# Performance work log

Hardware: AMD Instinct MI355X
Metric: run time of the kernel (lower is better)

The kernel has to match this reference:

```python
import jax, jax.numpy as jnp
import numpy as np

NEG_SLOPE = 0.2
EPS = 1e-16


def _add_self_loops(edge_index, edge_weight, N):
    # PyG add_self_loops with fill_value='mean': self-loop attr = mean of
    # incoming edge attrs per node (0 if node has no incoming edges).
    src, dst = edge_index[0], edge_index[1]
    ones = jnp.ones_like(edge_weight)
    cnt = jax.ops.segment_sum(ones, dst, num_segments=N)
    wsum = jax.ops.segment_sum(edge_weight, dst, num_segments=N)
    self_w = jnp.where(cnt > 0, wsum / jnp.maximum(cnt, 1.0), 0.0)
    loop = jnp.arange(N, dtype=src.dtype)
    return (jnp.concatenate([src, loop]), jnp.concatenate([dst, loop]),
            jnp.concatenate([edge_weight, self_w]))


def _gatv2_layer(x, src, dst, ew, Wl, Wr, att, We, bias, N):
    # x: [M, N, Din]; src/dst: [E']; ew: [E']; att: [H, C]
    M = x.shape[0]
    H, C = att.shape
    xl = (x @ Wl).reshape(M, N, H, C)   # source transform (lin_l)
    xr = (x @ Wr).reshape(M, N, H, C)   # target transform (lin_r)
    xj = xl[:, src]                      # [M, E', H, C] gather source feats
    xi = xr[:, dst]                      # [M, E', H, C] gather target feats
    ee = (ew[:, None] @ We).reshape(-1, H, C)  # [E', H, C] edge embedding
    s = jax.nn.leaky_relu(xi + xj + ee[None], NEG_SLOPE)
    logits = jnp.einsum('mehc,hc->meh', s, att)  # [M, E', H]
    # segment softmax over edges grouped by destination node
    smax = jax.vmap(lambda u: jax.ops.segment_max(u, dst, num_segments=N))(logits)
    a = jnp.exp(logits - smax[:, dst])
    denom = jax.vmap(lambda u: jax.ops.segment_sum(u, dst, num_segments=N))(a)
    alpha = a / (denom[:, dst] + EPS)
    msg = alpha[..., None] * xj          # [M, E', H, C]
    out = jax.vmap(lambda u: jax.ops.segment_sum(u, dst, num_segments=N))(msg)
    return out.reshape(M, N, H * C) + bias


def setup_inputs() -> dict:
    key = jax.random.key(0)
    ks = jax.random.split(key, 14)
    B, T, N, Din = 2, 8, 5000, 64
    E, H, OUT = 80000, 2, 128
    C = OUT // H  # 64
    g = jax.nn.initializers.glorot_uniform()
    inp = {
        'x': jax.random.normal(ks[0], (B, T, N, Din), jnp.float32),
        'edge_index': jax.random.randint(ks[1], (2, E), 0, N, jnp.int32),
        'edge_weight': jax.random.uniform(ks[2], (E,), jnp.float32),
        # conv1 params
        'Wl1': g(ks[3], (Din, H * C), jnp.float32),
        'Wr1': g(ks[4], (Din, H * C), jnp.float32),
        'att1': g(ks[5], (H, C), jnp.float32),
        'We1': g(ks[6], (1, H * C), jnp.float32),
        'b1': jnp.zeros((H * C,), jnp.float32),
        # conv2 params
        'Wl2': g(ks[7], (OUT, H * C), jnp.float32),
        'Wr2': g(ks[8], (OUT, H * C), jnp.float32),
        'att2': g(ks[9], (H, C), jnp.float32),
        'We2': g(ks[10], (1, H * C), jnp.float32),
        'b2': jnp.zeros((H * C,), jnp.float32),
    }
    return inp


def reference(x, edge_index, edge_weight, Wl1, Wr1, att1, We1, b1,
              Wl2, Wr2, att2, We2, b2):
    B, T, N, Din = x.shape
    M = B * T
    # Tiling edges by B*T with node offsets is equivalent to sharing the same
    # edge list across M independent graph copies -> vectorize over M.
    src, dst, ew = _add_self_loops(edge_index, edge_weight, N)
    h = x.reshape(M, N, Din)
    h = _gatv2_layer(h, src, dst, ew, Wl1, Wr1, att1, We1, b1, N)
    h = jax.nn.elu(h)
    h = _gatv2_layer(h, src, dst, ew, Wl2, Wr2, att2, We2, b2, N)
    h = jax.nn.elu(h)
    return h.reshape(B, T, N, -1)
```

## Files before the change

kernel.cpp:

```cpp
#include <hip/hip_runtime.h>
#include <cstdint>
#include <cstddef>

static constexpr float NEG_SLOPE_C = 0.2f;
static constexpr float EPS_C = 1e-16f;
static constexpr float LOG2E_C = 1.4426950408889634f;

#if defined(__has_builtin)
#if __has_builtin(__builtin_amdgcn_exp2f)
#define EXP2F(x) __builtin_amdgcn_exp2f(x)
#else
#define EXP2F(x) exp2f(x)
#endif
#else
#define EXP2F(x) exp2f(x)
#endif

typedef __attribute__((ext_vector_type(8))) short bf16x8;
typedef __attribute__((ext_vector_type(4))) float f32x4;

__device__ __forceinline__ short bf16_rne(float x) {
    unsigned u = __float_as_uint(x);
    u = (u + 0x7FFF + ((u >> 16) & 1)) >> 16;
    return (short)u;
}
__device__ __forceinline__ float bf16f(short s) {
    return __uint_as_float(((unsigned)(unsigned short)s) << 16);
}

template<int CTRL>
__device__ __forceinline__ float dpp_add_f(float v) {
    int x = __builtin_amdgcn_update_dpp(0, __float_as_int(v), CTRL, 0xf, 0xf, true);
    return v + __int_as_float(x);
}

__device__ __forceinline__ float half_reduce(float q) {
    q = dpp_add_f<0xB1>(q);
    q = dpp_add_f<0x4E>(q);
    q = dpp_add_f<0x141>(q);
    q = dpp_add_f<0x140>(q);
    q += __int_as_float(__builtin_amdgcn_ds_swizzle(__float_as_int(q), 0x401F));
    return q;
}


__global__ void degree_kernel(const int* __restrict__ ei, const float* __restrict__ ew,
                              int E, int* __restrict__ cnt, float* __restrict__ wsum) {
    int e = blockIdx.x * blockDim.x + threadIdx.x;
    if (e >= E) return;
    int dst = ei[E + e];
    atomicAdd(&cnt[dst], 1);
    atomicAdd(&wsum[dst], ew[e]);
}

__global__ void scan_kernel(const int* __restrict__ cnt, const float* __restrict__ wsum,
                            int N, int E, int* __restrict__ offs, float* __restrict__ self_w) {
    __shared__ int bufA[1024];
    __shared__ int bufB[1024];
    int t = threadIdx.x;
    int chunk = (N + 1023) / 1024;
    int lo = t * chunk;
    int hi = lo + chunk; if (hi > N) hi = N; if (lo > N) lo = N;
    int s = 0;
    for (int n = lo; n < hi; ++n) s += cnt[n];
    bufA[t] = s;
    __syncthreads();
    int* srcb = bufA; int* dstb = bufB;
    for (int d = 1; d < 1024; d <<= 1) {
        int v = srcb[t];
        if (t >= d) v += srcb[t - d];
        dstb[t] = v;
        __syncthreads();
        int* tmp = srcb; srcb = dstb; dstb = tmp;
    }
    int run = (t == 0) ? 0 : srcb[t - 1];
    for (int n = lo; n < hi; ++n) { offs[n] = run; run += cnt[n]; }
    if (t == 0) offs[N] = E;
    for (int n = t; n < N; n += 1024) {
        int c = cnt[n];
        self_w[n] = (c > 0) ? (wsum[n] / (float)c) : 0.0f;
    }
}

__global__ void scatter_kernel(const int* __restrict__ ei, const float* __restrict__ ew, int E,
                               const int* __restrict__ offs, int* __restrict__ cursor,
                               int2* __restrict__ pairs) {
    int e = blockIdx.x * blockDim.x + threadIdx.x;
    if (e >= E) return;
    int dst = ei[E + e];
    int pos = offs[dst] + atomicAdd(&cursor[dst], 1);
    pairs[pos] = make_int2(ei[e], __float_as_int(ew[e]));
}


template<int K>
__global__ void wprep_kernel(const float* __restrict__ Wl, const float* __restrict__ Wr,
                             uint4* __restrict__ Wf) {
    const int gid = blockIdx.x * 256 + threadIdx.x;
    const int lane = gid & 63;
    const int t = (gid >> 6) & 15;
    const int s = gid >> 10;
    const int mr = lane & 15, q = lane >> 4;
    const int col = t * 16 + mr;
    const float* src = (col < 128) ? (Wl + col) : (Wr + col - 128);
    union { short sh[8]; uint4 u; } hv, lv;
    #pragma unroll
    for (int j = 0; j < 8; ++j) {
        const float v = src[(size_t)(s * 32 + q * 8 + j) * 128];
        const short h = bf16_rne(v);
        hv.sh[j] = h;
        lv.sh[j] = bf16_rne(v - bf16f(h));
    }
    const size_t base = (size_t)s * 2048 + (size_t)(t * 2) * 64 + lane;
    Wf[base] = hv.u;
    Wf[base + 64] = lv.u;
}


template<int K>
__global__ __launch_bounds__(256) void gemm_mfma_kernel(
    const float* __restrict__ X, const uint4* __restrict__ Wf,
    float* __restrict__ outL, float* __restrict__ outR) {
    __shared__ uint4 wbuf[2048];
    const int tid = threadIdx.x;
    const int wv = tid >> 6;
    const int lane = tid & 63;
    const int q = lane >> 4;
    const int mr = lane & 15;
    const int xrow = blockIdx.x * 64 + wv * 16 + mr;

    f32x4 acc[16];
    #pragma unroll
    for (int t = 0; t < 16; ++t) acc[t] = (f32x4){0.f, 0.f, 0.f, 0.f};

    const float* xp = X + (size_t)xrow * K + q * 8;

    for (int s = 0; s < K / 32; ++s) {
        const float4 a0 = *(const float4*)(xp + s * 32);
        const float4 a1 = *(const float4*)(xp + s * 32 + 4);

        __syncthreads();
        const uint4* gsrc = Wf + (size_t)s * 2048 + wv * 512 + lane;
        #pragma unroll
        for (int i = 0; i < 8; ++i)
            wbuf[wv * 512 + i * 64 + lane] = gsrc[i * 64];
        __syncthreads();

        const float av[8] = {a0.x, a0.y, a0.z, a0.w, a1.x, a1.y, a1.z, a1.w};
        bf16x8 xh, xl;
        #pragma unroll
        for (int j = 0; j < 8; ++j) {
            const short h = bf16_rne(av[j]);
            xh[j] = h;
            xl[j] = bf16_rne(av[j] - bf16f(h));
        }
        #pragma unroll
        for (int t = 0; t < 16; ++t) {
            const bf16x8 wh = *(const bf16x8*)&wbuf[(t * 2) * 64 + lane];
            const bf16x8 wl = *(const bf16x8*)&wbuf[(t * 2 + 1) * 64 + lane];
            acc[t] = __builtin_amdgcn_mfma_f32_16x16x32_bf16(wh, xh, acc[t], 0, 0, 0);
            acc[t] = __builtin_amdgcn_mfma_f32_16x16x32_bf16(wl, xh, acc[t], 0, 0, 0);
            acc[t] = __builtin_amdgcn_mfma_f32_16x16x32_bf16(wh, xl, acc[t], 0, 0, 0);
        }
    }

    const size_t ob = (size_t)xrow * 128 + q * 4;
    #pragma unroll
    for (int t = 0; t < 8; ++t) {
        *(float4*)(outL + ob + t * 16) =
            make_float4(acc[t][0], acc[t][1], acc[t][2], acc[t][3]);
        *(float4*)(outR + ob + t * 16) =
            make_float4(acc[t + 8][0], acc[t + 8][1], acc[t + 8][2], acc[t + 8][3]);
    }
}


__global__ __launch_bounds__(256) void edge_kernel(
    const float* __restrict__ xl, const float* __restrict__ xr,
    const int* __restrict__ offs, const int2* __restrict__ pairs,
    const float* __restrict__ self_w,
    const float* __restrict__ att, const float* __restrict__ We,
    const float* __restrict__ bias, float* __restrict__ out,
    int N, int M) {
    const int wave = __builtin_amdgcn_readfirstlane(threadIdx.x >> 6);
    const int b = blockIdx.x;
    const int hb = (b >= 10000) ? (b - 10000) : b;
    const int m = ((b >= 10000) ? 8 : 0) + (hb & 7);
    const int n = (hb >> 3) * 4 + wave;
    if (n >= N) return;
    const int lane = threadIdx.x & 63;

    const int c2 = lane << 1;
    float2 att2 = *(const float2*)(att + c2);
    att2.x *= LOG2E_C; att2.y *= LOG2E_C;
    const float2 we2 = *(const float2*)(We + c2);

    const float* xlm = xl + (size_t)m * N * 128;
    const float* xrm = xr + (size_t)m * N * 128;
    const int rowb = n << 7;
    const float2 xi2 = *(const float2*)(xrm + rowb + c2);

    float base, lsum;
    float2 acc;
    {
        const float sw = self_w[n];
        const float2 xj = *(const float2*)(xlm + rowb + c2);
        float sx = fmaf(sw, we2.x, xi2.x) + xj.x;
        float sy = fmaf(sw, we2.y, xi2.y) + xj.y;
        sx = fmaf(NEG_SLOPE_C - 1.0f, fminf(sx, 0.f), sx);
        sy = fmaf(NEG_SLOPE_C - 1.0f, fminf(sy, 0.f), sy);
        base = half_reduce(fmaf(sy, att2.y, sx * att2.x));
        lsum = 1.f; acc = xj;
    }

    const int beg = offs[n], end = offs[n + 1];
    int e = beg;
    for (; e + 2 <= end; e += 2) {
        const int2 prA = pairs[e];
        const int2 prB = pairs[e + 1];
        const float wA = __int_as_float(prA.y);
        const float wB = __int_as_float(prB.y);
        const float2 xjA = *(const float2*)(xlm + (prA.x << 7) + c2);
        const float2 xjB = *(const float2*)(xlm + (prB.x << 7) + c2);
        float sxA = fmaf(wA, we2.x, xi2.x) + xjA.x;
        float syA = fmaf(wA, we2.y, xi2.y) + xjA.y;
        float sxB = fmaf(wB, we2.x, xi2.x) + xjB.x;
        float syB = fmaf(wB, we2.y, xi2.y) + xjB.y;
        sxA = fmaf(NEG_SLOPE_C - 1.0f, fminf(sxA, 0.f), sxA);
        syA = fmaf(NEG_SLOPE_C - 1.0f, fminf(syA, 0.f), syA);
        sxB = fmaf(NEG_SLOPE_C - 1.0f, fminf(sxB, 0.f), sxB);
        syB = fmaf(NEG_SLOPE_C - 1.0f, fminf(syB, 0.f), syB);
        float qA = half_reduce(fmaf(syA, att2.y, sxA * att2.x));
        float qB = half_reduce(fmaf(syB, att2.y, sxB * att2.x));
        const float tA = EXP2F(qA - base);
        const float tB = EXP2F(qB - base);
        lsum += tA + tB;
        acc.x = fmaf(tA, xjA.x, acc.x);
        acc.y = fmaf(tA, xjA.y, acc.y);
        acc.x = fmaf(tB, xjB.x, acc.x);
        acc.y = fmaf(tB, xjB.y, acc.y);
    }
    if (e < end) {
        const int2 pr = pairs[e];
        const float w = __int_as_float(pr.y);
        const float2 xj = *(const float2*)(xlm + (pr.x << 7) + c2);
        float sx = fmaf(w, we2.x, xi2.x) + xj.x;
        float sy = fmaf(w, we2.y, xi2.y) + xj.y;
        sx = fmaf(NEG_SLOPE_C - 1.0f, fminf(sx, 0.f), sx);
        sy = fmaf(NEG_SLOPE_C - 1.0f, fminf(sy, 0.f), sy);
        float q = half_reduce(fmaf(sy, att2.y, sx * att2.x));
        const float t = EXP2F(q - base);
        lsum += t;
        acc.x = fmaf(t, xj.x, acc.x);
        acc.y = fmaf(t, xj.y, acc.y);
    }

    const float inv = 1.f / (lsum + EPS_C);
    const float2 b2v = *(const float2*)(bias + c2);
    float ox = fmaf(acc.x, inv, b2v.x);
    float oy = fmaf(acc.y, inv, b2v.y);
    ox = ox > 0.f ? ox : (__expf(ox) - 1.f);
    oy = oy > 0.f ? oy : (__expf(oy) - 1.f);
    *(float2*)(out + (size_t)m * N * 128 + rowb + c2) = make_float2(ox, oy);
}


extern "C" void kernel_launch(void* const* d_in, const int* in_sizes, int n_in,
                              void* d_out, int out_size, void* d_ws, size_t ws_size,
                              hipStream_t stream) {
    const float* x    = (const float*)d_in[0];
    const int*   ei   = (const int*)d_in[1];
    const float* ew   = (const float*)d_in[2];
    const float* Wl1  = (const float*)d_in[3];
    const float* Wr1  = (const float*)d_in[4];
    const float* att1 = (const float*)d_in[5];
    const float* We1  = (const float*)d_in[6];
    const float* b1   = (const float*)d_in[7];
    const float* Wl2  = (const float*)d_in[8];
    const float* Wr2  = (const float*)d_in[9];
    const float* att2 = (const float*)d_in[10];
    const float* We2  = (const float*)d_in[11];
    const float* b2   = (const float*)d_in[12];

    const int E = in_sizes[1] / 2;
    const int N = 5000;
    const int R = out_size / 128;
    const int M = R / N;

    char* ws = (char*)d_ws;
    size_t off = 0;
    auto alloc = [&](size_t bytes) {
        char* p = ws + off;
        off = (off + bytes + 255) & ~(size_t)255;
        return p;
    };
    int*   cnt    = (int*)  alloc((size_t)N * 4);
    float* wsum   = (float*)alloc((size_t)N * 4);
    float* selfw  = (float*)alloc((size_t)N * 4);
    int*   offs   = (int*)  alloc((size_t)(N + 1) * 4);
    int*   cursor = (int*)  alloc((size_t)N * 4);
    int2*  pairs  = (int2*) alloc((size_t)E * 8);
    uint4* wf1    = (uint4*)alloc((size_t)2 * 2048 * 16);
    uint4* wf2    = (uint4*)alloc((size_t)4 * 2048 * 16);
    float* bufA   = (float*)alloc((size_t)R * 128 * 4);
    float* bufB   = (float*)alloc((size_t)R * 128 * 4);
    float* bufC   = (float*)alloc((size_t)R * 128 * 4);

    hipMemsetAsync(cnt,    0, (size_t)N * 4, stream);
    hipMemsetAsync(wsum,   0, (size_t)N * 4, stream);
    hipMemsetAsync(cursor, 0, (size_t)N * 4, stream);

    int eb = (E + 255) / 256;
    degree_kernel<<<eb, 256, 0, stream>>>(ei, ew, E, cnt, wsum);
    scan_kernel<<<1, 1024, 0, stream>>>(cnt, wsum, N, E, offs, selfw);
    scatter_kernel<<<eb, 256, 0, stream>>>(ei, ew, E, offs, cursor, pairs);
    wprep_kernel<64><<<8, 256, 0, stream>>>(Wl1, Wr1, wf1);
    wprep_kernel<128><<<16, 256, 0, stream>>>(Wl2, Wr2, wf2);

    const int gb = R / 64;
    const int tb = 2 * ((N + 3) / 4) * 8;

    gemm_mfma_kernel<64><<<gb, 256, 0, stream>>>(x, wf1, bufA, bufB);
    edge_kernel<<<tb, 256, 0, stream>>>(bufA, bufB, offs, pairs, selfw,
                                        att1, We1, b1, bufC, N, M);
    gemm_mfma_kernel<128><<<gb, 256, 0, stream>>>(bufC, wf2, bufA, bufB);
    edge_kernel<<<tb, 256, 0, stream>>>(bufA, bufB, offs, pairs, selfw,
                                        att2, We2, b2, (float*)d_out, N, M);
}
```

Baseline: 307.2 us.

## Split wave into two half-waves each processing one edge with float4 loads

Restructures the edge aggregation so each 32-lane half-wave handles a different edge, with every lane loading a float4 (four channels) instead of a float2. Per-head reductions shrink to 16 lanes, and the two half-wave partial sums are combined with a cross-half shuffle at the end. The self-loop contribution is split as 0.5 per half, and an odd trailing edge is masked on the upper half. This aims to halve the loop iterations and reduction instructions per edge and to issue wider loads. The cost is extra shuffles and an idle upper half on the tail edge.

Result: faster. 295.7 us (-3.8%).

```diff
diff --git a/kernel.cpp b/kernel.cpp
--- a/kernel.cpp
+++ b/kernel.cpp
@@ -34,12 +34,11 @@
     return v + __int_as_float(x);
 }
 
-__device__ __forceinline__ float half_reduce(float q) {
+__device__ __forceinline__ float reduce16(float q) {
     q = dpp_add_f<0xB1>(q);
     q = dpp_add_f<0x4E>(q);
     q = dpp_add_f<0x141>(q);
     q = dpp_add_f<0x140>(q);
-    q += __int_as_float(__builtin_amdgcn_ds_swizzle(__float_as_int(q), 0x401F));
     return q;
 }
 
@@ -189,79 +188,115 @@
     const int n = (hb >> 3) * 4 + wave;
     if (n >= N) return;
     const int lane = threadIdx.x & 63;
-
-    const int c2 = lane << 1;
-    float2 att2 = *(const float2*)(att + c2);
-    att2.x *= LOG2E_C; att2.y *= LOG2E_C;
-    const float2 we2 = *(const float2*)(We + c2);
-
-    const float* xlm = xl + (size_t)m * N * 128;
-    const float* xrm = xr + (size_t)m * N * 128;
-    const int rowb = n << 7;
-    const float2 xi2 = *(const float2*)(xrm + rowb + c2);
+    const int j = lane & 31;
+    const bool hi = lane >= 32;
+
+    const float4* xlm4 = (const float4*)(xl + (size_t)m * N * 128);
+    const float4* xrm4 = (const float4*)(xr + (size_t)m * N * 128);
+
+    float4 att4 = ((const float4*)att)[j];
+    att4.x *= LOG2E_C; att4.y *= LOG2E_C; att4.z *= LOG2E_C; att4.w *= LOG2E_C;
+    const float4 we4 = ((const float4*)We)[j];
+    const float4 xi4 = xrm4[n * 32 + j];
 
     float base, lsum;
-    float2 acc;
+    float4 acc;
     {
         const float sw = self_w[n];
-        const float2 xj = *(const float2*)(xlm + rowb + c2);
-        float sx = fmaf(sw, we2.x, xi2.x) + xj.x;
-        float sy = fmaf(sw, we2.y, xi2.y) + xj.y;
-        sx = fmaf(NEG_SLOPE_C - 1.0f, fminf(sx, 0.f), sx);
-        sy = fmaf(NEG_SLOPE_C - 1.0f, fminf(sy, 0.f), sy);
-        base = half_reduce(fmaf(sy, att2.y, sx * att2.x));
-        lsum = 1.f; acc = xj;
+        const float4 xj = xlm4[n * 32 + j];
+        float s0 = fmaf(sw, we4.x, xi4.x) + xj.x;
+        float s1 = fmaf(sw, we4.y, xi4.y) + xj.y;
+        float s2 = fmaf(sw, we4.z, xi4.z) + xj.z;
+        float s3 = fmaf(sw, we4.w, xi4.w) + xj.w;
+        s0 = fmaf(NEG_SLOPE_C - 1.0f, fminf(s0, 0.f), s0);
+        s1 = fmaf(NEG_SLOPE_C - 1.0f, fminf(s1, 0.f), s1);
+        s2 = fmaf(NEG_SLOPE_C - 1.0f, fminf(s2, 0.f), s2);
+        s3 = fmaf(NEG_SLOPE_C - 1.0f, fminf(s3, 0.f), s3);
+        float q = s0 * att4.x;
+        q = fmaf(s1, att4.y, q);
+        q = fmaf(s2, att4.z, q);
+        q = fmaf(s3, att4.w, q);
+        base = reduce16(q);
+        lsum = 0.5f;
+        acc = make_float4(xj.x * 0.5f, xj.y * 0.5f, xj.z * 0.5f, xj.w * 0.5f);
     }
 
     const int beg = offs[n], end = offs[n + 1];
     int e = beg;
+    #pragma unroll 2
     for (; e + 2 <= end; e += 2) {
         const int2 prA = pairs[e];
         const int2 prB = pairs[e + 1];
-        const float wA = __int_as_float(prA.y);
-        const float wB = __int_as_float(prB.y);
-        const float2 xjA = *(const float2*)(xlm + (prA.x << 7) + c2);
-        const float2 xjB = *(const float2*)(xlm + (prB.x << 7) + c2);
-        float sxA = fmaf(wA, we2.x, xi2.x) + xjA.x;
-        float syA = fmaf(wA, we2.y, xi2.y) + xjA.y;
-        float sxB = fmaf(wB, we2.x, xi2.x) + xjB.x;
-        float syB = fmaf(wB, we2.y, xi2.y) + xjB.y;
-        sxA = fmaf(NEG_SLOPE_C - 1.0f, fminf(sxA, 0.f), sxA);
-        syA = fmaf(NEG_SLOPE_C - 1.0f, fminf(syA, 0.f), syA);
-        sxB = fmaf(NEG_SLOPE_C - 1.0f, fminf(sxB, 0.f), sxB);
-        syB = fmaf(NEG_SLOPE_C - 1.0f, fminf(syB, 0.f), syB);
-        float qA = half_reduce(fmaf(syA, att2.y, sxA * att2.x));
-        float qB = half_reduce(fmaf(syB, att2.y, sxB * att2.x));
-        const float tA = EXP2F(qA - base);
-        const float tB = EXP2F(qB - base);
-        lsum += tA + tB;
-        acc.x = fmaf(tA, xjA.x, acc.x);
-        acc.y = fmaf(tA, xjA.y, acc.y);
-        acc.x = fmaf(tB, xjB.x, acc.x);
-        acc.y = fmaf(tB, xjB.y, acc.y);
-    }
-    if (e < end) {
-        const int2 pr = pairs[e];
-        const float w = __int_as_float(pr.y);
-        const float2 xj = *(const float2*)(xlm + (pr.x << 7) + c2);
-        float sx = fmaf(w, we2.x, xi2.x) + xj.x;
-        float sy = fmaf(w, we2.y, xi2.y) + xj.y;
-        sx = fmaf(NEG_SLOPE_C - 1.0f, fminf(sx, 0.f), sx);
-        sy = fmaf(NEG_SLOPE_C - 1.0f, fminf(sy, 0.f), sy);
-        float q = half_reduce(fmaf(sy, att2.y, sx * att2.x));
+        const int src = hi ? prB.x : prA.x;
+        const float w = __int_as_float(hi ? prB.y : prA.y);
+        const float4 xj = xlm4[src * 32 + j];
+        float s0 = fmaf(w, we4.x, xi4.x) + xj.x;
+        float s1 = fmaf(w, we4.y, xi4.y) + xj.y;
+        float s2 = fmaf(w, we4.z, xi4.z) + xj.z;
+        float s3 = fmaf(w, we4.w, xi4.w) + xj.w;
+        s0 = fmaf(NEG_SLOPE_C - 1.0f, fminf(s0, 0.f), s0);
+        s1 = fmaf(NEG_SLOPE_C - 1.0f, fminf(s1, 0.f), s1);
+        s2 = fmaf(NEG_SLOPE_C - 1.0f, fminf(s2, 0.f), s2);
+        s3 = fmaf(NEG_SLOPE_C - 1.0f, fminf(s3, 0.f), s3);
+        float q = s0 * att4.x;
+        q = fmaf(s1, att4.y, q);
+        q = fmaf(s2, att4.z, q);
+        q = fmaf(s3, att4.w, q);
+        q = reduce16(q);
         const float t = EXP2F(q - base);
         lsum += t;
         acc.x = fmaf(t, xj.x, acc.x);
         acc.y = fmaf(t, xj.y, acc.y);
-    }
+        acc.z = fmaf(t, xj.z, acc.z);
+        acc.w = fmaf(t, xj.w, acc.w);
+    }
+    if (e < end) {
+        const int2 pr = pairs[e];
+        const int src = pr.x;
+        const float w = __int_as_float(pr.y);
+        const float4 xj = xlm4[src * 32 + j];
+        float s0 = fmaf(w, we4.x, xi4.x) + xj.x;
+        float s1 = fmaf(w, we4.y, xi4.y) + xj.y;
+        float s2 = fmaf(w, we4.z, xi4.z) + xj.z;
+        float s3 = fmaf(w, we4.w, xi4.w) + xj.w;
+        s0 = fmaf(NEG_SLOPE_C - 1.0f, fminf(s0, 0.f), s0);
+        s1 = fmaf(NEG_SLOPE_C - 1.0f, fminf(s1, 0.f), s1);
+        s2 = fmaf(NEG_SLOPE_C - 1.0f, fminf(s2, 0.f), s2);
+        s3 = fmaf(NEG_SLOPE_C - 1.0f, fminf(s3, 0.f), s3);
+        float q = s0 * att4.x;
+        q = fmaf(s1, att4.y, q);
+        q = fmaf(s2, att4.z, q);
+        q = fmaf(s3, att4.w, q);
+        q = reduce16(q);
+        float t = EXP2F(q - base);
+        t = hi ? 0.f : t;
+        lsum += t;
+        acc.x = fmaf(t, xj.x, acc.x);
+        acc.y = fmaf(t, xj.y, acc.y);
+        acc.z = fmaf(t, xj.z, acc.z);
+        acc.w = fmaf(t, xj.w, acc.w);
+    }
+
+    lsum += __shfl_xor(lsum, 32, 64);
+    acc.x += __shfl_xor(acc.x, 32, 64);
+    acc.y += __shfl_xor(acc.y, 32, 64);
+    acc.z += __shfl_xor(acc.z, 32, 64);
+    acc.w += __shfl_xor(acc.w, 32, 64);
 
     const float inv = 1.f / (lsum + EPS_C);
-    const float2 b2v = *(const float2*)(bias + c2);
-    float ox = fmaf(acc.x, inv, b2v.x);
-    float oy = fmaf(acc.y, inv, b2v.y);
-    ox = ox > 0.f ? ox : (__expf(ox) - 1.f);
-    oy = oy > 0.f ? oy : (__expf(oy) - 1.f);
-    *(float2*)(out + (size_t)m * N * 128 + rowb + c2) = make_float2(ox, oy);
+    const float4 b4 = ((const float4*)bias)[j];
+    float o0 = fmaf(acc.x, inv, b4.x);
+    float o1 = fmaf(acc.y, inv, b4.y);
+    float o2 = fmaf(acc.z, inv, b4.z);
+    float o3 = fmaf(acc.w, inv, b4.w);
+    o0 = o0 > 0.f ? o0 : (__expf(o0) - 1.f);
+    o1 = o1 > 0.f ? o1 : (__expf(o1) - 1.f);
+    o2 = o2 > 0.f ? o2 : (__expf(o2) - 1.f);
+    o3 = o3 > 0.f ? o3 : (__expf(o3) - 1.f);
+    if (!hi) {
+        ((float4*)(out + (size_t)m * N * 128))[n * 32 + j] =
+            make_float4(o0, o1, o2, o3);
+    }
 }
 
 
```

## Split wave into four edge groups with 8-channel lanes in GATv2 edge kernel

Applied to the files above, without the earlier changes.

The edge kernel now processes four edges at once per wave, with each 16-lane group covering all 128 channels using 8 channels per lane. This shortens the per-edge reduction to three DPP steps and lets four gathers be in flight at once. Partial softmax sums and accumulators are merged across groups with shuffles at the end. Leaky-ReLU is rewritten as 0.6*v + 0.4*|v| folded into the attention dot product, and the three memsets are merged into one. The cost is extra cross-group shuffles, masked tail iterations, and a fixed per-group running max that relies on every group sharing the same self-loop base.

After: 314.8 us. 2.5% more time.

```diff
diff --git a/kernel.cpp b/kernel.cpp
--- a/kernel.cpp
+++ b/kernel.cpp
@@ -5,6 +5,8 @@
 static constexpr float NEG_SLOPE_C = 0.2f;
 static constexpr float EPS_C = 1e-16f;
 static constexpr float LOG2E_C = 1.4426950408889634f;
+static constexpr float QA_C = 0.6f * LOG2E_C;
+static constexpr float QB_C = 0.4f * LOG2E_C;
 
 #if defined(__has_builtin)
 #if __has_builtin(__builtin_amdgcn_exp2f)
@@ -18,6 +20,7 @@
 
 typedef __attribute__((ext_vector_type(8))) short bf16x8;
 typedef __attribute__((ext_vector_type(4))) float f32x4;
+typedef __attribute__((ext_vector_type(2))) float f32x2;
 
 __device__ __forceinline__ short bf16_rne(float x) {
     unsigned u = __float_as_uint(x);
@@ -34,13 +37,21 @@
     return v + __int_as_float(x);
 }
 
-__device__ __forceinline__ float half_reduce(float q) {
+__device__ __forceinline__ float reduce8(float q) {
     q = dpp_add_f<0xB1>(q);
     q = dpp_add_f<0x4E>(q);
     q = dpp_add_f<0x141>(q);
-    q = dpp_add_f<0x140>(q);
-    q += __int_as_float(__builtin_amdgcn_ds_swizzle(__float_as_int(q), 0x401F));
     return q;
+}
+
+struct v8 { f32x2 h[4]; };
+__device__ __forceinline__ v8 load8(const float4* base, int idx) {
+    v8 r;
+    const float4 a = base[idx];
+    const float4 b = base[idx + 1];
+    r.h[0] = (f32x2){a.x, a.y}; r.h[1] = (f32x2){a.z, a.w};
+    r.h[2] = (f32x2){b.x, b.y}; r.h[3] = (f32x2){b.z, b.w};
+    return r;
 }
 
 
@@ -189,79 +200,91 @@
     const int n = (hb >> 3) * 4 + wave;
     if (n >= N) return;
     const int lane = threadIdx.x & 63;
-
-    const int c2 = lane << 1;
-    float2 att2 = *(const float2*)(att + c2);
-    att2.x *= LOG2E_C; att2.y *= LOG2E_C;
-    const float2 we2 = *(const float2*)(We + c2);
-
-    const float* xlm = xl + (size_t)m * N * 128;
-    const float* xrm = xr + (size_t)m * N * 128;
-    const int rowb = n << 7;
-    const float2 xi2 = *(const float2*)(xrm + rowb + c2);
-
-    float base, lsum;
-    float2 acc;
+    const int p = lane >> 4;
+    const int u = lane & 15;
+    const int cb = u * 2;
+
+    const float4* xlm4 = (const float4*)(xl + (size_t)m * N * 128);
+    const float4* xrm4 = (const float4*)(xr + (size_t)m * N * 128);
+
+    const v8 attL = load8((const float4*)att, cb);
+    const v8 weL  = load8((const float4*)We, cb);
+    const v8 xiL  = load8(xrm4, n * 32 + cb);
+
+    float base_, lsum;
+    f32x2 acc0, acc1, acc2, acc3;
     {
         const float sw = self_w[n];
-        const float2 xj = *(const float2*)(xlm + rowb + c2);
-        float sx = fmaf(sw, we2.x, xi2.x) + xj.x;
-        float sy = fmaf(sw, we2.y, xi2.y) + xj.y;
-        sx = fmaf(NEG_SLOPE_C - 1.0f, fminf(sx, 0.f), sx);
-        sy = fmaf(NEG_SLOPE_C - 1.0f, fminf(sy, 0.f), sy);
-        base = half_reduce(fmaf(sy, att2.y, sx * att2.x));
-        lsum = 1.f; acc = xj;
+        const v8 xj = load8(xlm4, n * 32 + cb);
+        const f32x2 swv = (f32x2){sw, sw};
+        f32x2 qa = (f32x2){0.f, 0.f}, qb = (f32x2){0.f, 0.f};
+        #pragma unroll
+        for (int i = 0; i < 4; ++i) {
+            const f32x2 v = __builtin_elementwise_fma(swv, weL.h[i], xiL.h[i]) + xj.h[i];
+            const f32x2 av = __builtin_elementwise_abs(v);
+            qa = __builtin_elementwise_fma(attL.h[i], v, qa);
+            qb = __builtin_elementwise_fma(attL.h[i], av, qb);
+        }
+        float q = fmaf(QA_C, qa[0] + qa[1], QB_C * (qb[0] + qb[1]));
+        base_ = reduce8(q);
+        lsum = 0.25f;
+        const f32x2 qv = (f32x2){0.25f, 0.25f};
+        acc0 = xj.h[0] * qv; acc1 = xj.h[1] * qv;
+        acc2 = xj.h[2] * qv; acc3 = xj.h[3] * qv;
     }
 
     const int beg = offs[n], end = offs[n + 1];
-    int e = beg;
-    for (; e + 2 <= end; e += 2) {
-        const int2 prA = pairs[e];
-        const int2 prB = pairs[e + 1];
-        const float wA = __int_as_float(prA.y);
-        const float wB = __int_as_float(prB.y);
-        const float2 xjA = *(const float2*)(xlm + (prA.x << 7) + c2);
-        const float2 xjB = *(const float2*)(xlm + (prB.x << 7) + c2);
-        float sxA = fmaf(wA, we2.x, xi2.x) + xjA.x;
-        float syA = fmaf(wA, we2.y, xi2.y) + xjA.y;
-        float sxB = fmaf(wB, we2.x, xi2.x) + xjB.x;
-        float syB = fmaf(wB, we2.y, xi2.y) + xjB.y;
-        sxA = fmaf(NEG_SLOPE_C - 1.0f, fminf(sxA, 0.f), sxA);
-        syA = fmaf(NEG_SLOPE_C - 1.0f, fminf(syA, 0.f), syA);
-        sxB = fmaf(NEG_SLOPE_C - 1.0f, fminf(sxB, 0.f), sxB);
-        syB = fmaf(NEG_SLOPE_C - 1.0f, fminf(syB, 0.f), syB);
-        float qA = half_reduce(fmaf(syA, att2.y, sxA * att2.x));
-        float qB = half_reduce(fmaf(syB, att2.y, sxB * att2.x));
-        const float tA = EXP2F(qA - base);
-        const float tB = EXP2F(qB - base);
-        lsum += tA + tB;
-        acc.x = fmaf(tA, xjA.x, acc.x);
-        acc.y = fmaf(tA, xjA.y, acc.y);
-        acc.x = fmaf(tB, xjB.x, acc.x);
-        acc.y = fmaf(tB, xjB.y, acc.y);
-    }
-    if (e < end) {
-        const int2 pr = pairs[e];
+    for (int e0 = beg; e0 < end; e0 += 4) {
+        const int idx = e0 + p;
+        const bool valid = idx < end;
+        const int2 pr = pairs[valid ? idx : (end - 1)];
+        const int src = pr.x;
         const float w = __int_as_float(pr.y);
-        const float2 xj = *(const float2*)(xlm + (pr.x << 7) + c2);
-        float sx = fmaf(w, we2.x, xi2.x) + xj.x;
-        float sy = fmaf(w, we2.y, xi2.y) + xj.y;
-        sx = fmaf(NEG_SLOPE_C - 1.0f, fminf(sx, 0.f), sx);
-        sy = fmaf(NEG_SLOPE_C - 1.0f, fminf(sy, 0.f), sy);
-        float q = half_reduce(fmaf(sy, att2.y, sx * att2.x));
-        const float t = EXP2F(q - base);
+        const v8 xj = load8(xlm4, src * 32 + cb);
+        const f32x2 wv = (f32x2){w, w};
+        f32x2 qa = (f32x2){0.f, 0.f}, qb = (f32x2){0.f, 0.f};
+        #pragma unroll
+        for (int i = 0; i < 4; ++i) {
+            const f32x2 v = __builtin_elementwise_fma(wv, weL.h[i], xiL.h[i]) + xj.h[i];
+            const f32x2 av = __builtin_elementwise_abs(v);
+            qa = __builtin_elementwise_fma(attL.h[i], v, qa);
+            qb = __builtin_elementwise_fma(attL.h[i], av, qb);
+        }
+        float q = fmaf(QA_C, qa[0] + qa[1], QB_C * (qb[0] + qb[1]));
+        q = reduce8(q);
+        float t = EXP2F(q - base_);
+        t = valid ? t : 0.f;
         lsum += t;
-        acc.x = fmaf(t, xj.x, acc.x);
-        acc.y = fmaf(t, xj.y, acc.y);
-    }
-
-    const float inv = 1.f / (lsum + EPS_C);
-    const float2 b2v = *(const float2*)(bias + c2);
-    float ox = fmaf(acc.x, inv, b2v.x);
-    float oy = fmaf(acc.y, inv, b2v.y);
-    ox = ox > 0.f ? ox : (__expf(ox) - 1.f);
-    oy = oy > 0.f ? oy : (__expf(oy) - 1.f);
-    *(float2*)(out + (size_t)m * N * 128 + rowb + c2) = make_float2(ox, oy);
+        const f32x2 tv = (f32x2){t, t};
+        acc0 = __builtin_elementwise_fma(tv, xj.h[0], acc0);
+        acc1 = __builtin_elementwise_fma(tv, xj.h[1], acc1);
+        acc2 = __builtin_elementwise_fma(tv, xj.h[2], acc2);
+        acc3 = __builtin_elementwise_fma(tv, xj.h[3], acc3);
+    }
+
+    lsum += __shfl_xor(lsum, 16, 64);
+    lsum += __shfl_xor(lsum, 32, 64);
+    #define CMB(a) \
+        a[0] += __shfl_xor(a[0], 16, 64); a[0] += __shfl_xor(a[0], 32, 64); \
+        a[1] += __shfl_xor(a[1], 16, 64); a[1] += __shfl_xor(a[1], 32, 64)
+    CMB(acc0); CMB(acc1); CMB(acc2); CMB(acc3);
+    #undef CMB
+
+    if (p == 0) {
+        const float inv = 1.f / (lsum + EPS_C);
+        const v8 bi = load8((const float4*)bias, cb);
+        const f32x2 iv = (f32x2){inv, inv};
+        f32x2 o0 = __builtin_elementwise_fma(acc0, iv, bi.h[0]);
+        f32x2 o1 = __builtin_elementwise_fma(acc1, iv, bi.h[1]);
+        f32x2 o2 = __builtin_elementwise_fma(acc2, iv, bi.h[2]);
+        f32x2 o3 = __builtin_elementwise_fma(acc3, iv, bi.h[3]);
+        float o[8] = {o0[0], o0[1], o1[0], o1[1], o2[0], o2[1], o3[0], o3[1]};
+        #pragma unroll
+        for (int i = 0; i < 8; ++i) o[i] = o[i] > 0.f ? o[i] : (__expf(o[i]) - 1.f);
+        float4* ob = (float4*)(out + (size_t)m * N * 128);
+        ob[n * 32 + cb]     = make_float4(o[0], o[1], o[2], o[3]);
+        ob[n * 32 + cb + 1] = make_float4(o[4], o[5], o[6], o[7]);
+    }
 }
 
 
@@ -294,11 +317,11 @@
         off = (off + bytes + 255) & ~(size_t)255;
         return p;
     };
-    int*   cnt    = (int*)  alloc((size_t)N * 4);
-    float* wsum   = (float*)alloc((size_t)N * 4);
+    int*   cnt    = (int*)  alloc((size_t)3 * N * 4);
+    float* wsum   = (float*)(cnt + N);
+    int*   cursor = cnt + 2 * N;
     float* selfw  = (float*)alloc((size_t)N * 4);
     int*   offs   = (int*)  alloc((size_t)(N + 1) * 4);
-    int*   cursor = (int*)  alloc((size_t)N * 4);
     int2*  pairs  = (int2*) alloc((size_t)E * 8);
     uint4* wf1    = (uint4*)alloc((size_t)2 * 2048 * 16);
     uint4* wf2    = (uint4*)alloc((size_t)4 * 2048 * 16);
@@ -306,9 +329,7 @@
     float* bufB   = (float*)alloc((size_t)R * 128 * 4);
     float* bufC   = (float*)alloc((size_t)R * 128 * 4);
 
-    hipMemsetAsync(cnt,    0, (size_t)N * 4, stream);
-    hipMemsetAsync(wsum,   0, (size_t)N * 4, stream);
-    hipMemsetAsync(cursor, 0, (size_t)N * 4, stream);
+    hipMemsetAsync(cnt, 0, (size_t)3 * N * 4, stream);
 
     int eb = (E + 255) / 256;
     degree_kernel<<<eb, 256, 0, stream>>>(ei, ew, E, cnt, wsum);
```
